# Kernel tuning notes

Hardware: AMD Instinct MI355X
Metric: run time of the kernel (lower is better)

The kernel has to match this reference:

```python
import jax, jax.numpy as jnp
import numpy as np
from jax import lax

B, C, H, W = 64, 3, 224, 224
P, NP, D, HEADS, DEPTH = 16, 196, 384, 6, 6
DD, DHEADS, DDEPTH = 256, 8, 4
NVIS = 49


def setup_inputs():
    key = jax.random.key(0)
    ks = iter(jax.random.split(key, 64))
    def rn(shape, s=0.02):
        return jax.random.normal(next(ks), shape, jnp.float32) * s
    perms = jax.vmap(lambda k: jax.random.permutation(k, NP))(jax.random.split(next(ks), B))
    inp = {
        'x': jax.random.normal(next(ks), (B, C, H, W), jnp.float32),
        'unmasked_idx': perms[:, :NVIS].astype(jnp.int32),
        'masked_idx': perms[:, NVIS:].astype(jnp.int32),
        'conv_w': rn((D, C, P, P)), 'conv_b': jnp.zeros((D,), jnp.float32),
        'cls_token': rn((D,)), 'pos_embed': rn((NP + 1, D)),
        'enc_ln1_w': jnp.ones((DEPTH, D), jnp.float32), 'enc_ln1_b': jnp.zeros((DEPTH, D), jnp.float32),
        'enc_qkv_w': rn((DEPTH, 3 * D, D)), 'enc_qkv_b': jnp.zeros((DEPTH, 3 * D), jnp.float32),
        'enc_out_w': rn((DEPTH, D, D)), 'enc_out_b': jnp.zeros((DEPTH, D), jnp.float32),
        'enc_ln2_w': jnp.ones((DEPTH, D), jnp.float32), 'enc_ln2_b': jnp.zeros((DEPTH, D), jnp.float32),
        'enc_fc1_w': rn((DEPTH, 4 * D, D)), 'enc_fc1_b': jnp.zeros((DEPTH, 4 * D), jnp.float32),
        'enc_fc2_w': rn((DEPTH, D, 4 * D)), 'enc_fc2_b': jnp.zeros((DEPTH, D), jnp.float32),
        'enc_norm_w': jnp.ones((D,), jnp.float32), 'enc_norm_b': jnp.zeros((D,), jnp.float32),
        'dec_embed_w': rn((DD, D)), 'dec_embed_b': jnp.zeros((DD,), jnp.float32),
        'mask_token': rn((DD,)), 'dec_pos_embed': rn((NP + 1, DD)),
        'dec_ln1_w': jnp.ones((DDEPTH, DD), jnp.float32), 'dec_ln1_b': jnp.zeros((DDEPTH, DD), jnp.float32),
        'dec_qkv_w': rn((DDEPTH, 3 * DD, DD)), 'dec_qkv_b': jnp.zeros((DDEPTH, 3 * DD), jnp.float32),
        'dec_out_w': rn((DDEPTH, DD, DD)), 'dec_out_b': jnp.zeros((DDEPTH, DD), jnp.float32),
        'dec_ln2_w': jnp.ones((DDEPTH, DD), jnp.float32), 'dec_ln2_b': jnp.zeros((DDEPTH, DD), jnp.float32),
        'dec_fc1_w': rn((DDEPTH, 4 * DD, DD)), 'dec_fc1_b': jnp.zeros((DDEPTH, 4 * DD), jnp.float32),
        'dec_fc2_w': rn((DDEPTH, DD, 4 * DD)), 'dec_fc2_b': jnp.zeros((DDEPTH, DD), jnp.float32),
        'dec_norm_w': jnp.ones((DD,), jnp.float32), 'dec_norm_b': jnp.zeros((DD,), jnp.float32),
        'pred_w': rn((P * P * 3, DD)), 'pred_b': jnp.zeros((P * P * 3,), jnp.float32),
    }
    return inp


def layer_norm(x, w, b, eps=1e-5):
    m = x.mean(-1, keepdims=True)
    v = ((x - m) ** 2).mean(-1, keepdims=True)
    return (x - m) * lax.rsqrt(v + eps) * w + b


def mha(x, wqkv, bqkv, wo, bo, h):
    b, s, d = x.shape
    dh = d // h
    qkv = x @ wqkv.T + bqkv
    q, k, v = jnp.split(qkv, 3, axis=-1)
    sp = lambda t: t.reshape(b, s, h, dh).transpose(0, 2, 1, 3)  # [b,h,s,dh]
    q, k, v = sp(q), sp(k), sp(v)
    scores = jnp.einsum('bhqd,bhkd->bhqk', q, k) * (1.0 / np.sqrt(dh))
    a = jax.nn.softmax(scores, axis=-1)
    o = jnp.einsum('bhqk,bhkd->bhqd', a, v).transpose(0, 2, 1, 3).reshape(b, s, d)
    return o @ wo.T + bo


def run_blocks(x, depth, heads, ln1_w, ln1_b, qkv_w, qkv_b, out_w, out_b, ln2_w, ln2_b, fc1_w, fc1_b, fc2_w, fc2_b):
    for i in range(depth):
        x = x + mha(layer_norm(x, ln1_w[i], ln1_b[i]), qkv_w[i], qkv_b[i], out_w[i], out_b[i], heads)
        hdn = jax.nn.gelu(layer_norm(x, ln2_w[i], ln2_b[i]) @ fc1_w[i].T + fc1_b[i], approximate=False)
        x = x + hdn @ fc2_w[i].T + fc2_b[i]
    return x


def reference(x, unmasked_idx, masked_idx, conv_w, conv_b, cls_token, pos_embed,
              enc_ln1_w, enc_ln1_b, enc_qkv_w, enc_qkv_b, enc_out_w, enc_out_b,
              enc_ln2_w, enc_ln2_b, enc_fc1_w, enc_fc1_b, enc_fc2_w, enc_fc2_b,
              enc_norm_w, enc_norm_b, dec_embed_w, dec_embed_b, mask_token, dec_pos_embed,
              dec_ln1_w, dec_ln1_b, dec_qkv_w, dec_qkv_b, dec_out_w, dec_out_b,
              dec_ln2_w, dec_ln2_b, dec_fc1_w, dec_fc1_b, dec_fc2_w, dec_fc2_b,
              dec_norm_w, dec_norm_b, pred_w, pred_b):
    b = x.shape[0]
    # patch embed: conv stride=kernel=16 -> [B, D, 14, 14] -> [B, 196, D]
    p = lax.conv_general_dilated(x, conv_w, (P, P), 'VALID',
                                 dimension_numbers=('NCHW', 'OIHW', 'NCHW'))
    p = p.reshape(b, D, NP).transpose(0, 2, 1) + conv_b + pos_embed[1:]
    bi = jnp.arange(b)[:, None]
    vis = p[bi, unmasked_idx]                      # [B, NVIS, D] per-sample gather
    cls = cls_token + pos_embed[0]
    xe = jnp.concatenate([jnp.broadcast_to(cls, (b, 1, D)), vis], axis=1)
    xe = run_blocks(xe, DEPTH, HEADS, enc_ln1_w, enc_ln1_b, enc_qkv_w, enc_qkv_b,
                    enc_out_w, enc_out_b, enc_ln2_w, enc_ln2_b, enc_fc1_w, enc_fc1_b,
                    enc_fc2_w, enc_fc2_b)
    xe = layer_norm(xe, enc_norm_w, enc_norm_b)
    xd = xe @ dec_embed_w.T + dec_embed_b          # [B, 1+NVIS, DD]
    vis_dec = xd[:, 1:, :]                         # drop cls
    full = jnp.zeros((b, NP, DD), xd.dtype)
    full = full.at[bi, unmasked_idx].set(vis_dec)  # scatter visible tokens
    full = full.at[bi, masked_idx].set(mask_token) # scatter mask tokens
    full = full + dec_pos_embed[1:]
    xf = run_blocks(full, DDEPTH, DHEADS, dec_ln1_w, dec_ln1_b, dec_qkv_w, dec_qkv_b,
                    dec_out_w, dec_out_b, dec_ln2_w, dec_ln2_b, dec_fc1_w, dec_fc1_b,
                    dec_fc2_w, dec_fc2_b)
    xf = layer_norm(xf, dec_norm_w, dec_norm_b)
    return xf @ pred_w.T + pred_b                  # [B, NP, P*P*3]
```

## Files before the change

### kernel.cpp

```cpp
#include <hip/hip_runtime.h>
#include <hip/hip_bf16.h>

#define B_    64
#define NP_   196
#define NVIS_ 49
#define D_    384
#define DD_   256
#define SENC_ 50
#define SDEC_ 196

typedef __hip_bfloat16 bf16;
typedef __attribute__((ext_vector_type(8))) short short8;
typedef __attribute__((ext_vector_type(4))) float float4v;

__device__ __forceinline__ float bf2f(bf16 x) { return __bfloat162float(x); }
__device__ __forceinline__ bf16 f2bf(float x) { return __float2bfloat16(x); }
__device__ __forceinline__ float rdin(const void* p, long i, int f) {
  return f ? ((const float*)p)[i] : bf2f(((const bf16*)p)[i]);
}
__device__ __forceinline__ void gll16(const bf16* g, bf16* l) {
  __builtin_amdgcn_global_load_lds(
      (const __attribute__((address_space(1))) unsigned int*)g,
      (__attribute__((address_space(3))) unsigned int*)l, 16, 0, 0);
}

__global__ void probe_kernel(const void* w, int* flag) {
  int tid = threadIdx.x;
  float mx = 0.f;
  for (int i = tid; i < 512; i += 64)
    mx = fmaxf(mx, fabsf(bf2f(((const bf16*)w)[i])));
#pragma unroll
  for (int off = 32; off; off >>= 1) mx = fmaxf(mx, __shfl_xor(mx, off));
  if (tid == 0) *flag = (mx > 1e3f) ? 1 : 0;
}

__global__ __launch_bounds__(256) void fill_kernel(bf16* out, float v, int n) {
  int idx = blockIdx.x * 256 + threadIdx.x;
  if (idx < n) out[idx] = f2bf(v);
}

struct WLs { const void* s[11]; long d[11]; int n[11]; };
__global__ __launch_bounds__(256) void wconv_kernel(WLs L, bf16* Wb,
                                                    const int* dflag) {
  int f = *dflag;
  int seg = blockIdx.y;
  long n8 = (long)(L.n[seg] >> 3);
  long i = (long)blockIdx.x * 256 + threadIdx.x;
  if (i >= n8) return;
  bf16* d = Wb + L.d[seg] + i * 8;
  if (f) {
    const float4* s = (const float4*)L.s[seg] + i * 2;
    float4 a = s[0], b = s[1];
    union { uint4 u; bf16 h[8]; } pk;
    pk.h[0] = f2bf(a.x); pk.h[1] = f2bf(a.y); pk.h[2] = f2bf(a.z); pk.h[3] = f2bf(a.w);
    pk.h[4] = f2bf(b.x); pk.h[5] = f2bf(b.y); pk.h[6] = f2bf(b.z); pk.h[7] = f2bf(b.w);
    *(uint4*)d = pk.u;
  } else {
    *(uint4*)d = ((const uint4*)L.s[seg])[i];
  }
}

__global__ __launch_bounds__(256) void im2col_vis_kernel(
    const void* __restrict__ x, const int* __restrict__ unmasked,
    bf16* __restrict__ out, const int* __restrict__ dflag) {
  int f = *dflag;
  int idx = blockIdx.x * 256 + threadIdx.x;
  const int TOT = B_ * NVIS_ * 768;
  if (idx >= TOT) return;
  int k = idx % 768;
  int row = idx / 768;
  int j = row % NVIS_;
  int b = row / NVIS_;
  int n = unmasked[b * NVIS_ + j];
  int ph = n / 14, pw = n % 14;
  int c  = k >> 8;
  int rr = (k >> 4) & 15;
  int cc = k & 15;
  out[idx] = f2bf(rdin(x, (long)(((b * 3 + c) * 224) + ph * 16 + rr) * 224 + pw * 16 + cc, f));
}

#define UNR _Pragma("unroll")
template <int MODE, int TMW, int TNW>
__global__ __launch_bounds__(256) void gemm_kernel(
    const bf16* __restrict__ A, const bf16* __restrict__ W,
    const void* __restrict__ bias, long bOff,
    void* __restrict__ C, int M, int N, int K, int KS, int out_mode,
    const int* __restrict__ dflag) {
  constexpr int BM = 2 * TMW, BN = 2 * TNW;
  constexpr int AM = TMW / 16, AN = TNW / 16;
  constexpr int ACH = BM / 32, BCH = BN / 32;
  int f = *dflag;
  __shared__ bf16 Asl[2][BM * 64];
  __shared__ bf16 Bsl[2][BN * 64];
  int tid = threadIdx.x;

  int gx = gridDim.x;
  int nwg = gx * gridDim.y;
  int orig = blockIdx.y * gx + blockIdx.x;
  int q = nwg >> 3, rr_ = nwg & 7, xcd = orig & 7, off = orig >> 3;
  int wgid = (xcd < rr_ ? xcd * (q + 1) : rr_ * (q + 1) + (xcd - rr_) * q) + off;
  int bx = wgid % gx, by = wgid / gx, bz = blockIdx.z;

  int w = tid >> 6, lane = tid & 63;
  int quad = lane >> 4, l16 = lane & 15;
  int rb = l16 & 7;
  int wm = (w & 1) * TMW, wn = (w >> 1) * TNW;
  int srow = tid >> 3;
  int dcol = (tid & 7) * 8;
  int scol = (((tid & 7) ^ (srow & 7))) * 8;
  const bf16* Ab = A + (long)by * BM * K;
  const bf16* Wp = W + (long)bx * BN * K;
  int k0lo = bz * KS;

  float4v acc[AM][AN];
#pragma unroll
  for (int i = 0; i < AM; i++)
#pragma unroll
    for (int j = 0; j < AN; j++) acc[i][j] = (float4v){0.f, 0.f, 0.f, 0.f};

#define STAGE(buf, k0) \
  UNR for (int i_ = 0; i_ < ACH; i_++) { \
    int r_ = i_ * 32 + srow; \
    gll16(Ab + (long)r_ * K + (k0) + scol, &Asl[buf][r_ * 64 + dcol]); } \
  UNR for (int i_ = 0; i_ < BCH; i_++) { \
    int r_ = i_ * 32 + srow; \
    gll16(Wp + (long)r_ * K + (k0) + scol, &Bsl[buf][r_ * 64 + dcol]); }

#define COMPUTE(cur) UNR for (int kk = 0; kk < 2; kk++) { \
    short8 af[AM], bfr[AN]; \
    UNR for (int mi = 0; mi < AM; mi++) \
      af[mi] = *(const short8*)&Asl[cur][(wm + mi * 16 + l16) * 64 + ((kk * 4 + quad) ^ rb) * 8]; \
    UNR for (int ni = 0; ni < AN; ni++) \
      bfr[ni] = *(const short8*)&Bsl[cur][(wn + ni * 16 + l16) * 64 + ((kk * 4 + quad) ^ rb) * 8]; \
    UNR for (int mi = 0; mi < AM; mi++) \
      UNR for (int ni = 0; ni < AN; ni++) \
        acc[mi][ni] = __builtin_amdgcn_mfma_f32_16x16x32_bf16( \
            af[mi], bfr[ni], acc[mi][ni], 0, 0, 0); }

  STAGE(0, k0lo);
  __syncthreads();
  int nst = KS >> 6;
  for (int s = 0; s < nst; s++) {
    int cur = s & 1;
    if (s + 1 < nst) STAGE(cur ^ 1, k0lo + (s + 1) * 64);
    COMPUTE(cur);
    __syncthreads();
  }
#undef STAGE
#undef COMPUTE

  int om = (out_mode == 2) ? (f ? 1 : 0) : out_mode;
  float* Cf = (float*)C + (long)bz * M * N;
  bf16*  Cb = (bf16*)C;
#pragma unroll
  for (int mi = 0; mi < AM; mi++) {
#pragma unroll
    for (int ni = 0; ni < AN; ni++) {
      int cn = bx * BN + wn + ni * 16 + l16;
      float bval = (bz == 0) ? rdin(bias, bOff + cn, f) : 0.f;
#pragma unroll
      for (int r = 0; r < 4; r++) {
        int cm = by * BM + wm + mi * 16 + quad * 4 + r;
        float v = acc[mi][ni][r] + bval;
        if constexpr (MODE == 1) v = 0.5f * v * (1.0f + erff(v * 0.70710678f));
        if (om) Cf[(long)cm * N + cn] = v;
        else    Cb[(long)cm * N + cn] = f2bf(v);
      }
    }
  }
}

template <int N>
__global__ __launch_bounds__(256) void ln_kernel(
    float* __restrict__ X, const float* __restrict__ G0,
    const float* __restrict__ G1, const float* __restrict__ G2,
    const void* __restrict__ w, long wOff, const void* __restrict__ bv,
    long bOff, bf16* __restrict__ Y, int M, const int* __restrict__ dflag) {
  int f = *dflag;
  int row = blockIdx.x * 4 + (threadIdx.x >> 6);
  int lane = threadIdx.x & 63;
  if (row >= M) return;
  float* xr = X + (long)row * N;
  const float* g0 = G0 ? G0 + (long)row * N : nullptr;
  const float* g1 = G1 ? G1 + (long)row * N : nullptr;
  const float* g2 = G2 ? G2 + (long)row * N : nullptr;
  constexpr int CNT = N / 64;
  float v[CNT];
  float sum = 0.f;
#pragma unroll
  for (int i = 0; i < CNT; i++) {
    int c = lane + 64 * i;
    float t = xr[c];
    if (g0) t += g0[c];
    if (g1) t += g1[c];
    if (g2) t += g2[c];
    if (g0) xr[c] = t;
    v[i] = t;
    sum += t;
  }
#pragma unroll
  for (int off = 32; off; off >>= 1) sum += __shfl_xor(sum, off);
  float mean = sum * (1.0f / N);
  float vs = 0.f;
#pragma unroll
  for (int i = 0; i < CNT; i++) { float d = v[i] - mean; vs += d * d; }
#pragma unroll
  for (int off = 32; off; off >>= 1) vs += __shfl_xor(vs, off);
  float rstd = rsqrtf(vs * (1.0f / N) + 1e-5f);
  bf16* yr = Y + (long)row * N;
#pragma unroll
  for (int i = 0; i < CNT; i++) {
    int cidx = lane + 64 * i;
    yr[cidx] = f2bf((v[i] - mean) * rstd * rdin(w, wOff + cidx, f) + rdin(bv, bOff + cidx, f));
  }
}

__global__ __launch_bounds__(256) void attn_dec_kernel(
    const bf16* __restrict__ qkv, bf16* __restrict__ out) {
  const int S = SDEC_, DH = 32, Dm = 256, tri = 768;
  const int KLD = 40, VLD = 232, PLD = 232;
  int b = blockIdx.x >> 3, h = blockIdx.x & 7;
  __shared__ bf16 Ksh[208 * KLD];
  __shared__ bf16 Vt[32 * VLD];
  __shared__ bf16 Psh[4][16 * PLD];
  int tid = threadIdx.x;
  const bf16* base = qkv + (long)b * S * tri;
  for (int idx = tid; idx < S * 4; idx += 256) {
    int s = idx >> 2, part = (idx & 3) * 8;
    uint4 v = *(const uint4*)(base + (long)s * tri + Dm + h * DH + part);
    *(uint4*)(&Ksh[s * KLD + part]) = v;
  }
  if (tid < 12 * 4) {
    int s = 196 + (tid >> 2), part = (tid & 3) * 8;
    uint4 z = {0, 0, 0, 0};
    *(uint4*)(&Ksh[s * KLD + part]) = z;
  }
  for (int idx = tid; idx < S * DH; idx += 256) {
    int s = idx >> 5, d = idx & 31;
    Vt[d * VLD + s] = base[(long)s * tri + 2 * Dm + h * DH + d];
  }
  for (int idx = tid; idx < 32 * 36; idx += 256) {
    int d = idx / 36, c = 196 + idx % 36;
    Vt[d * VLD + c] = f2bf(0.f);
  }
  __syncthreads();
  int w = tid >> 6, lane = tid & 63, l16 = lane & 15, quad = lane >> 4;
  bf16* Pw = &Psh[w][0];
  const float scale = 0.17677669529663687f;
  for (int qt = w; qt < 13; qt += 4) {
    int q0 = qt * 16;
    int qr = min(q0 + l16, S - 1);
    short8 qf = *(const short8*)(base + (long)qr * tri + h * DH + quad * 8);
    float4v sc[13];
#pragma unroll
    for (int t = 0; t < 13; t++) {
      short8 kf = *(const short8*)&Ksh[(t * 16 + l16) * KLD + quad * 8];
      sc[t] = __builtin_amdgcn_mfma_f32_16x16x32_bf16(
          qf, kf, (float4v){0.f, 0.f, 0.f, 0.f}, 0, 0, 0);
    }
    float mx[4] = {-1e30f, -1e30f, -1e30f, -1e30f};
#pragma unroll
    for (int t = 0; t < 13; t++) {
      bool valid = (t * 16 + l16) < S;
#pragma unroll
      for (int r = 0; r < 4; r++) {
        float v = valid ? sc[t][r] * scale : -1e30f;
        sc[t][r] = v;
        mx[r] = fmaxf(mx[r], v);
      }
    }
#pragma unroll
    for (int off = 1; off < 16; off <<= 1)
#pragma unroll
      for (int r = 0; r < 4; r++) mx[r] = fmaxf(mx[r], __shfl_xor(mx[r], off));
    float sm[4] = {0.f, 0.f, 0.f, 0.f};
#pragma unroll
    for (int t = 0; t < 13; t++)
#pragma unroll
      for (int r = 0; r < 4; r++) {
        float p = __expf(sc[t][r] - mx[r]);
        sc[t][r] = p;
        sm[r] += p;
      }
#pragma unroll
    for (int off = 1; off < 16; off <<= 1)
#pragma unroll
      for (int r = 0; r < 4; r++) sm[r] += __shfl_xor(sm[r], off);
#pragma unroll
    for (int t = 0; t < 14; t++) {
      int col = t * 16 + l16;
#pragma unroll
      for (int r = 0; r < 4; r++) {
        float p = (t < 13) ? sc[t][r] : 0.f;
        Pw[(quad * 4 + r) * PLD + col] = f2bf(p);
      }
    }
    __asm__ volatile("s_waitcnt lgkmcnt(0)" ::: "memory");
    float4v o0 = {0.f, 0.f, 0.f, 0.f}, o1 = {0.f, 0.f, 0.f, 0.f};
#pragma unroll
    for (int kc = 0; kc < 7; kc++) {
      short8 pf = *(const short8*)&Pw[l16 * PLD + kc * 32 + quad * 8];
      short8 v0 = *(const short8*)&Vt[l16 * VLD + kc * 32 + quad * 8];
      short8 v1 = *(const short8*)&Vt[(16 + l16) * VLD + kc * 32 + quad * 8];
      o0 = __builtin_amdgcn_mfma_f32_16x16x32_bf16(pf, v0, o0, 0, 0, 0);
      o1 = __builtin_amdgcn_mfma_f32_16x16x32_bf16(pf, v1, o1, 0, 0, 0);
    }
#pragma unroll
    for (int r = 0; r < 4; r++) {
      int row = q0 + quad * 4 + r;
      if (row < S) {
        float inv = 1.f / sm[r];
        bf16* op = out + ((long)(b * S + row)) * Dm + h * DH;
        op[l16]      = f2bf(o0[r] * inv);
        op[16 + l16] = f2bf(o1[r] * inv);
      }
    }
  }
}

__global__ __launch_bounds__(128) void attn_enc_kernel(
    const bf16* __restrict__ qkv, bf16* __restrict__ out) {
  const int S = SENC_, H = 6, DH = 64, Dm = H * DH, tri = 3 * Dm;
  int b = blockIdx.x / H, h = blockIdx.x % H;
  int tid = threadIdx.x;
  __shared__ float Ks[SENC_ * 64];
  __shared__ float Vs[SENC_ * 64];
  __shared__ float P1[SENC_ * 66];
  const bf16* base = qkv + (long)b * S * tri;
  for (int idx = tid; idx < S * 8; idx += 128) {
    int s = idx >> 3, part = (idx & 7) * 8;
    union { uint4 u; bf16 hh[8]; } kk, vv;
    kk.u = *(const uint4*)(base + (long)s * tri + Dm + h * DH + part);
    vv.u = *(const uint4*)(base + (long)s * tri + 2 * Dm + h * DH + part);
#pragma unroll
    for (int j = 0; j < 8; j++) {
      Ks[s * DH + part + j] = bf2f(kk.hh[j]);
      Vs[s * DH + part + j] = bf2f(vv.hh[j]);
    }
  }
  __syncthreads();
  int w = tid >> 6, lane = tid & 63;
  int row = lane;
  float q[DH], o[DH];
  float m = -1e30f, l = 0.f;
  if (lane < S) {
    const float scale = 0.125f;
#pragma unroll
    for (int d = 0; d < DH; d++) {
      q[d] = bf2f(base[(long)row * tri + h * DH + d]) * scale;
      o[d] = 0.f;
    }
    int jlo = w * 25, jhi = jlo + 25;
    for (int j = jlo; j < jhi; j++) {
      float s = 0.f;
#pragma unroll
      for (int d = 0; d < DH; d++) s += q[d] * Ks[j * DH + d];
      float mn = fmaxf(m, s);
      float corr = __expf(m - mn);
      float p = __expf(s - mn);
      l = l * corr + p;
      m = mn;
#pragma unroll
      for (int d = 0; d < DH; d++) o[d] = o[d] * corr + p * Vs[j * DH + d];
    }
    if (w == 1) {
#pragma unroll
      for (int d = 0; d < DH; d++) P1[row * 66 + d] = o[d];
      P1[row * 66 + 64] = m;
      P1[row * 66 + 65] = l;
    }
  }
  __syncthreads();
  if (w == 0 && lane < S) {
    float m1 = P1[row * 66 + 64], l1 = P1[row * 66 + 65];
    float mg = fmaxf(m, m1);
    float e0 = __expf(m - mg), e1 = __expf(m1 - mg);
    float lg = l * e0 + l1 * e1;
    float inv = 1.f / lg;
    bf16* op = out + ((long)(b * S + row) * Dm + h * DH);
#pragma unroll
    for (int d = 0; d < DH; d++)
      op[d] = f2bf((o[d] * e0 + P1[row * 66 + d] * e1) * inv);
  }
}

__global__ __launch_bounds__(256) void build_xe_kernel(
    const float* __restrict__ G0, const float* __restrict__ G1,
    const float* __restrict__ G2, const void* __restrict__ cls,
    const void* __restrict__ pos, const int* __restrict__ unmasked,
    float* __restrict__ xe, const int* __restrict__ dflag) {
  int f = *dflag;
  int idx = blockIdx.x * 256 + threadIdx.x;
  const int TOT = B_ * SENC_ * D_;
  if (idx >= TOT) return;
  int d = idx % D_;
  int s = (idx / D_) % SENC_;
  int b = idx / (D_ * SENC_);
  float v;
  if (s == 0) {
    v = rdin(cls, d, f) + rdin(pos, d, f);
  } else {
    int j = s - 1;
    int n = unmasked[b * NVIS_ + j];
    long r = (long)(b * NVIS_ + j) * D_ + d;
    v = G0[r] + G1[r] + G2[r] + rdin(pos, (long)(1 + n) * D_ + d, f);
  }
  xe[idx] = v;
}

__global__ __launch_bounds__(256) void dec_init_kernel(
    const void* __restrict__ mask_token, const void* __restrict__ dpos,
    float* __restrict__ full, const int* __restrict__ dflag) {
  int f = *dflag;
  int idx = blockIdx.x * 256 + threadIdx.x;
  const int TOT = B_ * NP_ * DD_;
  if (idx >= TOT) return;
  int d = idx % DD_;
  int n = (idx / DD_) % NP_;
  full[idx] = rdin(mask_token, d, f) + rdin(dpos, (long)(1 + n) * DD_ + d, f);
}

__global__ __launch_bounds__(256) void dec_scatter_kernel(
    const float* __restrict__ Gx0, const float* __restrict__ Gx1,
    const int* __restrict__ unmasked, const void* __restrict__ dpos,
    float* __restrict__ full, const int* __restrict__ dflag) {
  int f = *dflag;
  int idx = blockIdx.x * 256 + threadIdx.x;
  const int TOT = B_ * NVIS_ * DD_;
  if (idx >= TOT) return;
  int d = idx % DD_;
  int j = (idx / DD_) % NVIS_;
  int b = idx / (DD_ * NVIS_);
  int n = unmasked[b * NVIS_ + j];
  long r = (long)(b * SENC_ + 1 + j) * DD_ + d;
  full[((long)(b * NP_ + n)) * DD_ + d] =
      Gx0[r] + Gx1[r] + rdin(dpos, (long)(1 + n) * DD_ + d, f);
}

extern "C" void kernel_launch(void* const* d_in, const int* in_sizes, int n_in,
                              void* d_out, int out_size, void* d_ws, size_t ws_size,
                              hipStream_t stream) {
  (void)in_sizes; (void)n_in;
  const int* unmasked = (const int*)d_in[1];
  const int M_ENC = B_ * SENC_;
  const int M_DEC = B_ * NP_;

  const size_t NEEDED = 87588880;
  if (ws_size < NEEDED) {
    fill_kernel<<<(out_size + 255) / 256, 256, 0, stream>>>(
        (bf16*)d_out, (float)(ws_size >> 20), out_size);
    return;
  }
  char* wsb = (char*)d_ws;
  bf16*  big    = (bf16*)wsb;
  float* full   = (float*)(wsb + 25690112);
  bf16*  im2col = (bf16*)(wsb + 25690112);
  bf16*  t0     = (bf16*)(wsb + 38535168);
  float* xe     = (float*)(wsb + 44957696);
  float* Gdec   = (float*)(wsb + 44957696);
  int*   dflag  = (int*)(wsb + 58884096);
  bf16*  Wb     = (bf16*)(wsb + 58884112);
  float* Gp0 = (float*)(wsb + 0);
  float* Gp1 = (float*)(wsb + 4915200);
  float* Gp2 = (float*)(wsb + 9830400);
  float* Gf0 = (float*)(wsb + 9830400);
  float* Gf1 = (float*)(wsb + 14745600);
  float* Gf2 = (float*)(wsb + 19660800);
  float* Gx0 = (float*)(wsb + 0);
  float* Gx1 = (float*)(wsb + 3276800);

  const long o_conv = 0,        o_eqkv = 294912,  o_eout = 2949120;
  const long o_efc1 = 3833856,  o_efc2 = 7372800, o_demb = 10911744;
  const long o_dqkv = 11010048, o_dout = 11796480, o_dfc1 = 12058624;
  const long o_dfc2 = 13107200, o_pred = 14155776;

  probe_kernel<<<1, 64, 0, stream>>>(d_in[3], dflag);
  {
    WLs L;
    L.s[0] = d_in[3];  L.d[0] = o_conv; L.n[0] = 294912;
    L.s[1] = d_in[9];  L.d[1] = o_eqkv; L.n[1] = 2654208;
    L.s[2] = d_in[11]; L.d[2] = o_eout; L.n[2] = 884736;
    L.s[3] = d_in[15]; L.d[3] = o_efc1; L.n[3] = 3538944;
    L.s[4] = d_in[17]; L.d[4] = o_efc2; L.n[4] = 3538944;
    L.s[5] = d_in[21]; L.d[5] = o_demb; L.n[5] = 98304;
    L.s[6] = d_in[27]; L.d[6] = o_dqkv; L.n[6] = 786432;
    L.s[7] = d_in[29]; L.d[7] = o_dout; L.n[7] = 262144;
    L.s[8] = d_in[33]; L.d[8] = o_dfc1; L.n[8] = 1048576;
    L.s[9] = d_in[35]; L.d[9] = o_dfc2; L.n[9] = 1048576;
    L.s[10] = d_in[39]; L.d[10] = o_pred; L.n[10] = 196608;
    dim3 g((3538944 / 8 + 255) / 256, 11);
    wconv_kernel<<<g, 256, 0, stream>>>(L, Wb, dflag);
  }

  auto gemm = [&](int mode, int cfg, const bf16* A, const bf16* Wp,
                  const void* bias, long bOff, void* C,
                  int M, int N, int K, int splits, int out_mode) {
    int BM = (cfg == 2) ? 64 : 128;
    dim3 g(N / 64, M / BM, splits);
    int KS = K / splits;
    if (mode == 0) {
      if (cfg == 1) gemm_kernel<0, 64, 32><<<g, 256, 0, stream>>>(A, Wp, bias, bOff, C, M, N, K, KS, out_mode, dflag);
      else          gemm_kernel<0, 32, 32><<<g, 256, 0, stream>>>(A, Wp, bias, bOff, C, M, N, K, KS, out_mode, dflag);
    } else {
      if (cfg == 1) gemm_kernel<1, 64, 32><<<g, 256, 0, stream>>>(A, Wp, bias, bOff, C, M, N, K, KS, out_mode, dflag);
      else          gemm_kernel<1, 32, 32><<<g, 256, 0, stream>>>(A, Wp, bias, bOff, C, M, N, K, KS, out_mode, dflag);
    }
  };

  {
    int tot = B_ * NVIS_ * 768;
    im2col_vis_kernel<<<(tot + 255) / 256, 256, 0, stream>>>(d_in[0], unmasked, im2col, dflag);
    gemm(0, 2, im2col, Wb + o_conv, d_in[4], 0, Gp0, 3200, D_, 768, 3, 1);
    int tot2 = B_ * SENC_ * D_;
    build_xe_kernel<<<(tot2 + 255) / 256, 256, 0, stream>>>(
        Gp0, Gp1, Gp2, d_in[5], d_in[6], unmasked, xe, dflag);
  }

  const float *eg0 = nullptr, *eg1 = nullptr, *eg2 = nullptr;
  for (int i = 0; i < 6; i++) {
    ln_kernel<D_><<<M_ENC / 4, 256, 0, stream>>>(
        xe, eg0, eg1, eg2, d_in[7], (long)i * D_, d_in[8], (long)i * D_, t0, M_ENC, dflag);
    gemm(0, 2, t0, Wb + o_eqkv + (long)i * 3 * D_ * D_, d_in[10], (long)i * 3 * D_, big, M_ENC, 3 * D_, D_, 1, 0);
    attn_enc_kernel<<<B_ * 6, 128, 0, stream>>>(big, t0);
    gemm(0, 2, t0, Wb + o_eout + (long)i * D_ * D_, d_in[12], (long)i * D_, Gp0, M_ENC, D_, D_, 2, 1);
    ln_kernel<D_><<<M_ENC / 4, 256, 0, stream>>>(
        xe, Gp0, Gp1, nullptr, d_in[13], (long)i * D_, d_in[14], (long)i * D_, t0, M_ENC, dflag);
    gemm(1, 2, t0, Wb + o_efc1 + (long)i * 4 * D_ * D_, d_in[16], (long)i * 4 * D_, big, M_ENC, 4 * D_, D_, 1, 0);
    gemm(0, 2, big, Wb + o_efc2 + (long)i * D_ * 4 * D_, d_in[18], (long)i * D_, Gf0, M_ENC, D_, 4 * D_, 3, 1);
    eg0 = Gf0; eg1 = Gf1; eg2 = Gf2;
  }
  ln_kernel<D_><<<M_ENC / 4, 256, 0, stream>>>(
      xe, Gf0, Gf1, Gf2, d_in[19], 0, d_in[20], 0, t0, M_ENC, dflag);
  gemm(0, 2, t0, Wb + o_demb, d_in[22], 0, Gx0, M_ENC, DD_, D_, 2, 1);

  {
    int tot = B_ * NP_ * DD_;
    dec_init_kernel<<<(tot + 255) / 256, 256, 0, stream>>>(d_in[23], d_in[24], full, dflag);
    int tot2 = B_ * NVIS_ * DD_;
    dec_scatter_kernel<<<(tot2 + 255) / 256, 256, 0, stream>>>(
        Gx0, Gx1, unmasked, d_in[24], full, dflag);
  }

  const float* dg = nullptr;
  for (int i = 0; i < 4; i++) {
    ln_kernel<DD_><<<M_DEC / 4, 256, 0, stream>>>(
        full, dg, nullptr, nullptr, d_in[25], (long)i * DD_, d_in[26], (long)i * DD_, t0, M_DEC, dflag);
    gemm(0, 1, t0, Wb + o_dqkv + (long)i * 3 * DD_ * DD_, d_in[28], (long)i * 3 * DD_, big, M_DEC, 3 * DD_, DD_, 1, 0);
    attn_dec_kernel<<<B_ * 8, 256, 0, stream>>>(big, t0);
    gemm(0, 2, t0, Wb + o_dout + (long)i * DD_ * DD_, d_in[30], (long)i * DD_, Gdec, M_DEC, DD_, DD_, 1, 1);
    ln_kernel<DD_><<<M_DEC / 4, 256, 0, stream>>>(
        full, Gdec, nullptr, nullptr, d_in[31], (long)i * DD_, d_in[32], (long)i * DD_, t0, M_DEC, dflag);
    gemm(1, 1, t0, Wb + o_dfc1 + (long)i * 4 * DD_ * DD_, d_in[34], (long)i * 4 * DD_, big, M_DEC, 4 * DD_, DD_, 1, 0);
    gemm(0, 2, big, Wb + o_dfc2 + (long)i * DD_ * 4 * DD_, d_in[36], (long)i * DD_, Gdec, M_DEC, DD_, 4 * DD_, 1, 1);
    dg = Gdec;
  }
  ln_kernel<DD_><<<M_DEC / 4, 256, 0, stream>>>(
      full, Gdec, nullptr, nullptr, d_in[37], 0, d_in[38], 0, t0, M_DEC, dflag);

  gemm(0, 1, t0, Wb + o_pred, d_in[40], 0, d_out, M_DEC, 768, DD_, 1, 2);
}
```

Baseline: 1.261 ms.

## Add residual-fused GEMM epilogue, larger tile config, and finer vmcnt-based pipelining

The GEMM kernel gains a MODE 2 epilogue that adds a float residual in place, so the decoder out-proj and fc2 write straight into the residual stream and the following layernorm no longer reads a separate delta buffer. A new 128x128 tile config is added and several GEMMs are switched to larger tiles to improve operand reuse. The main-loop sync is changed from __syncthreads to explicit s_waitcnt vmcnt counts plus raw barriers, so the compute on the current buffer can overlap the in-flight async LDS loads for the next one. The in-place read-then-write of the residual is safe only because each element is read and written by the same thread, and larger tiles cut the number of workgroups, which may hurt occupancy for the smaller M sizes.

```diff
diff --git a/kernel.cpp b/kernel.cpp
--- a/kernel.cpp
+++ b/kernel.cpp
@@ -22,6 +22,12 @@
   __builtin_amdgcn_global_load_lds(
       (const __attribute__((address_space(1))) unsigned int*)g,
       (__attribute__((address_space(3))) unsigned int*)l, 16, 0, 0);
+}
+template <int N> __device__ __forceinline__ void waitcnt_vm() {
+  if constexpr (N == 0) asm volatile("s_waitcnt vmcnt(0)" ::: "memory");
+  else if constexpr (N == 4) asm volatile("s_waitcnt vmcnt(4)" ::: "memory");
+  else if constexpr (N == 6) asm volatile("s_waitcnt vmcnt(6)" ::: "memory");
+  else if constexpr (N == 8) asm volatile("s_waitcnt vmcnt(8)" ::: "memory");
 }
 
 __global__ void probe_kernel(const void* w, int* flag) {
@@ -83,12 +89,13 @@
 template <int MODE, int TMW, int TNW>
 __global__ __launch_bounds__(256) void gemm_kernel(
     const bf16* __restrict__ A, const bf16* __restrict__ W,
-    const void* __restrict__ bias, long bOff,
+    const void* __restrict__ bias, long bOff, const float* __restrict__ res,
     void* __restrict__ C, int M, int N, int K, int KS, int out_mode,
     const int* __restrict__ dflag) {
   constexpr int BM = 2 * TMW, BN = 2 * TNW;
   constexpr int AM = TMW / 16, AN = TNW / 16;
   constexpr int ACH = BM / 32, BCH = BN / 32;
+  constexpr int VW = ACH + BCH;
   int f = *dflag;
   __shared__ bf16 Asl[2][BM * 64];
   __shared__ bf16 Bsl[2][BN * 64];
@@ -138,13 +145,20 @@
             af[mi], bfr[ni], acc[mi][ni], 0, 0, 0); }
 
   STAGE(0, k0lo);
-  __syncthreads();
+  asm volatile("s_waitcnt vmcnt(0)" ::: "memory");
+  __builtin_amdgcn_s_barrier();
   int nst = KS >> 6;
   for (int s = 0; s < nst; s++) {
     int cur = s & 1;
-    if (s + 1 < nst) STAGE(cur ^ 1, k0lo + (s + 1) * 64);
+    if (s + 1 < nst) {
+      STAGE(cur ^ 1, k0lo + (s + 1) * 64);
+      waitcnt_vm<VW>();
+    } else {
+      asm volatile("s_waitcnt vmcnt(0)" ::: "memory");
+    }
+    __builtin_amdgcn_s_barrier();
     COMPUTE(cur);
-    __syncthreads();
+    if (s + 1 < nst) __builtin_amdgcn_s_barrier();
   }
 #undef STAGE
 #undef COMPUTE
@@ -163,6 +177,7 @@
         int cm = by * BM + wm + mi * 16 + quad * 4 + r;
         float v = acc[mi][ni][r] + bval;
         if constexpr (MODE == 1) v = 0.5f * v * (1.0f + erff(v * 0.70710678f));
+        if constexpr (MODE == 2) v += res[(long)cm * N + cn];
         if (om) Cf[(long)cm * N + cn] = v;
         else    Cb[(long)cm * N + cn] = f2bf(v);
       }
@@ -457,7 +472,6 @@
   bf16*  im2col = (bf16*)(wsb + 25690112);
   bf16*  t0     = (bf16*)(wsb + 38535168);
   float* xe     = (float*)(wsb + 44957696);
-  float* Gdec   = (float*)(wsb + 44957696);
   int*   dflag  = (int*)(wsb + 58884096);
   bf16*  Wb     = (bf16*)(wsb + 58884112);
   float* Gp0 = (float*)(wsb + 0);
@@ -493,24 +507,28 @@
   }
 
   auto gemm = [&](int mode, int cfg, const bf16* A, const bf16* Wp,
-                  const void* bias, long bOff, void* C,
+                  const void* bias, long bOff, const float* res, void* C,
                   int M, int N, int K, int splits, int out_mode) {
     int BM = (cfg == 2) ? 64 : 128;
-    dim3 g(N / 64, M / BM, splits);
+    int BN = (cfg == 0) ? 128 : 64;
+    dim3 g(N / BN, M / BM, splits);
     int KS = K / splits;
+#define GL(MO, TM, TN) gemm_kernel<MO, TM, TN><<<g, 256, 0, stream>>>( \
+        A, Wp, bias, bOff, res, C, M, N, K, KS, out_mode, dflag)
     if (mode == 0) {
-      if (cfg == 1) gemm_kernel<0, 64, 32><<<g, 256, 0, stream>>>(A, Wp, bias, bOff, C, M, N, K, KS, out_mode, dflag);
-      else          gemm_kernel<0, 32, 32><<<g, 256, 0, stream>>>(A, Wp, bias, bOff, C, M, N, K, KS, out_mode, dflag);
+      if (cfg == 0) GL(0, 64, 64); else if (cfg == 1) GL(0, 64, 32); else GL(0, 32, 32);
+    } else if (mode == 1) {
+      if (cfg == 0) GL(1, 64, 64); else if (cfg == 1) GL(1, 64, 32); else GL(1, 32, 32);
     } else {
-      if (cfg == 1) gemm_kernel<1, 64, 32><<<g, 256, 0, stream>>>(A, Wp, bias, bOff, C, M, N, K, KS, out_mode, dflag);
-      else          gemm_kernel<1, 32, 32><<<g, 256, 0, stream>>>(A, Wp, bias, bOff, C, M, N, K, KS, out_mode, dflag);
-    }
+      if (cfg == 0) GL(2, 64, 64); else if (cfg == 1) GL(2, 64, 32); else GL(2, 32, 32);
+    }
+#undef GL
   };
 
   {
     int tot = B_ * NVIS_ * 768;
     im2col_vis_kernel<<<(tot + 255) / 256, 256, 0, stream>>>(d_in[0], unmasked, im2col, dflag);
-    gemm(0, 2, im2col, Wb + o_conv, d_in[4], 0, Gp0, 3200, D_, 768, 3, 1);
+    gemm(0, 2, im2col, Wb + o_conv, d_in[4], 0, nullptr, Gp0, 3200, D_, 768, 3, 1);
     int tot2 = B_ * SENC_ * D_;
     build_xe_kernel<<<(tot2 + 255) / 256, 256, 0, stream>>>(
         Gp0, Gp1, Gp2, d_in[5], d_in[6], unmasked, xe, dflag);
@@ -520,18 +538,18 @@
   for (int i = 0; i < 6; i++) {
     ln_kernel<D_><<<M_ENC / 4, 256, 0, stream>>>(
         xe, eg0, eg1, eg2, d_in[7], (long)i * D_, d_in[8], (long)i * D_, t0, M_ENC, dflag);
-    gemm(0, 2, t0, Wb + o_eqkv + (long)i * 3 * D_ * D_, d_in[10], (long)i * 3 * D_, big, M_ENC, 3 * D_, D_, 1, 0);
+    gemm(0, 1, t0, Wb + o_eqkv + (long)i * 3 * D_ * D_, d_in[10], (long)i * 3 * D_, nullptr, big, M_ENC, 3 * D_, D_, 1, 0);
     attn_enc_kernel<<<B_ * 6, 128, 0, stream>>>(big, t0);
-    gemm(0, 2, t0, Wb + o_eout + (long)i * D_ * D_, d_in[12], (long)i * D_, Gp0, M_ENC, D_, D_, 2, 1);
+    gemm(0, 2, t0, Wb + o_eout + (long)i * D_ * D_, d_in[12], (long)i * D_, nullptr, Gp0, M_ENC, D_, D_, 2, 1);
     ln_kernel<D_><<<M_ENC / 4, 256, 0, stream>>>(
         xe, Gp0, Gp1, nullptr, d_in[13], (long)i * D_, d_in[14], (long)i * D_, t0, M_ENC, dflag);
-    gemm(1, 2, t0, Wb + o_efc1 + (long)i * 4 * D_ * D_, d_in[16], (long)i * 4 * D_, big, M_ENC, 4 * D_, D_, 1, 0);
-    gemm(0, 2, big, Wb + o_efc2 + (long)i * D_ * 4 * D_, d_in[18], (long)i * D_, Gf0, M_ENC, D_, 4 * D_, 3, 1);
+    gemm(1, 0, t0, Wb + o_efc1 + (long)i * 4 * D_ * D_, d_in[16], (long)i * 4 * D_, nullptr, big, M_ENC, 4 * D_, D_, 1, 0);
+    gemm(0, 2, big, Wb + o_efc2 + (long)i * D_ * 4 * D_, d_in[18], (long)i * D_, nullptr, Gf0, M_ENC, D_, 4 * D_, 3, 1);
     eg0 = Gf0; eg1 = Gf1; eg2 = Gf2;
   }
   ln_kernel<D_><<<M_ENC / 4, 256, 0, stream>>>(
       xe, Gf0, Gf1, Gf2, d_in[19], 0, d_in[20], 0, t0, M_ENC, dflag);
-  gemm(0, 2, t0, Wb + o_demb, d_in[22], 0, Gx0, M_ENC, DD_, D_, 2, 1);
+  gemm(0, 2, t0, Wb + o_demb, d_in[22], 0, nullptr, Gx0, M_ENC, DD_, D_, 2, 1);
 
   {
     int tot = B_ * NP_ * DD_;
@@ -541,21 +559,19 @@
         Gx0, Gx1, unmasked, d_in[24], full, dflag);
   }
 
-  const float* dg = nullptr;
   for (int i = 0; i < 4; i++) {
     ln_kernel<DD_><<<M_DEC / 4, 256, 0, stream>>>(
-        full, dg, nullptr, nullptr, d_in[25], (long)i * DD_, d_in[26], (long)i * DD_, t0, M_DEC, dflag);
-    gemm(0, 1, t0, Wb + o_dqkv + (long)i * 3 * DD_ * DD_, d_in[28], (long)i * 3 * DD_, big, M_DEC, 3 * DD_, DD_, 1, 0);
+        full, nullptr, nullptr, nullptr, d_in[25], (long)i * DD_, d_in[26], (long)i * DD_, t0, M_DEC, dflag);
+    gemm(0, 0, t0, Wb + o_dqkv + (long)i * 3 * DD_ * DD_, d_in[28], (long)i * 3 * DD_, nullptr, big, M_DEC, 3 * DD_, DD_, 1, 0);
     attn_dec_kernel<<<B_ * 8, 256, 0, stream>>>(big, t0);
-    gemm(0, 2, t0, Wb + o_dout + (long)i * DD_ * DD_, d_in[30], (long)i * DD_, Gdec, M_DEC, DD_, DD_, 1, 1);
+    gemm(2, 1, t0, Wb + o_dout + (long)i * DD_ * DD_, d_in[30], (long)i * DD_, full, full, M_DEC, DD_, DD_, 1, 1);
     ln_kernel<DD_><<<M_DEC / 4, 256, 0, stream>>>(
-        full, Gdec, nullptr, nullptr, d_in[31], (long)i * DD_, d_in[32], (long)i * DD_, t0, M_DEC, dflag);
-    gemm(1, 1, t0, Wb + o_dfc1 + (long)i * 4 * DD_ * DD_, d_in[34], (long)i * 4 * DD_, big, M_DEC, 4 * DD_, DD_, 1, 0);
-    gemm(0, 2, big, Wb + o_dfc2 + (long)i * DD_ * 4 * DD_, d_in[36], (long)i * DD_, Gdec, M_DEC, DD_, 4 * DD_, 1, 1);
-    dg = Gdec;
+        full, nullptr, nullptr, nullptr, d_in[31], (long)i * DD_, d_in[32], (long)i * DD_, t0, M_DEC, dflag);
+    gemm(1, 0, t0, Wb + o_dfc1 + (long)i * 4 * DD_ * DD_, d_in[34], (long)i * 4 * DD_, nullptr, big, M_DEC, 4 * DD_, DD_, 1, 0);
+    gemm(2, 1, big, Wb + o_dfc2 + (long)i * DD_ * 4 * DD_, d_in[36], (long)i * DD_, full, full, M_DEC, DD_, 4 * DD_, 1, 1);
   }
   ln_kernel<DD_><<<M_DEC / 4, 256, 0, stream>>>(
-      full, Gdec, nullptr, nullptr, d_in[37], 0, d_in[38], 0, t0, M_DEC, dflag);
-
-  gemm(0, 1, t0, Wb + o_pred, d_in[40], 0, d_out, M_DEC, 768, DD_, 1, 2);
-}
+      full, nullptr, nullptr, nullptr, d_in[37], 0, d_in[38], 0, t0, M_DEC, dflag);
+
+  gemm(0, 0, t0, Wb + o_pred, d_in[40], 0, nullptr, d_out, M_DEC, 768, DD_, 1, 2);
+}
```

Result: slower. 1.370 ms (+8.6%).
